# Performance work log

Hardware: AMD Instinct MI355X
Metric: run time of the kernel (lower is better)

Reference implementation:

```python
import jax, jax.numpy as jnp
import numpy as np

B, L, I, O, H = 128, 1024, 256, 256, 1024


def setup_inputs() -> dict:
    key = jax.random.key(0)
    ks = jax.random.split(key, 7)
    s = 1.0 / np.sqrt(H)  # torch LSTM/Linear init scale
    u = lambda k, shape: jax.random.uniform(k, shape, jnp.float32, -s, s)
    return {
        "trg": jax.random.normal(ks[0], (B, L, I), jnp.float32),
        "w_ih": u(ks[1], (4 * H, I)),
        "w_hh": u(ks[2], (4 * H, H)),
        "b_ih": u(ks[3], (4 * H,)),
        "b_hh": u(ks[4], (4 * H,)),
        "w_out": u(ks[5], (O, H)),
        "b_out": u(ks[6], (O,)),
    }


def reference(trg, w_ih, w_hh, b_ih, b_hh, w_out, b_out):
    # trg: [B, L, I] -> time-major [L, B, I]
    trg_t = jnp.transpose(trg, (1, 0, 2))
    # teacher_forcing_ratio = 1.0: step t consumes trg[t-1] (step 0 consumes trg[0])
    x_seq = jnp.concatenate([trg_t[:1], trg_t[:-1]], axis=0)  # [L, B, I]
    hdim = w_hh.shape[1]
    # precompute input-to-gate projection for all steps: [L, B, 4H]
    xp = jnp.einsum('lbi,gi->lbg', x_seq, w_ih) + b_ih + b_hh

    def step(carry, xp_t):
        h, c = carry
        z = xp_t + h @ w_hh.T  # [B, 4H]
        i_g, f_g, g_g, o_g = jnp.split(z, 4, axis=-1)  # torch gate order i,f,g,o
        c = jax.nn.sigmoid(f_g) * c + jax.nn.sigmoid(i_g) * jnp.tanh(g_g)
        h = jax.nn.sigmoid(o_g) * jnp.tanh(c)
        return (h, c), h

    bsz = trg.shape[0]
    h0 = jnp.zeros((bsz, hdim), trg.dtype)
    c0 = jnp.zeros((bsz, hdim), trg.dtype)
    _, hs = jax.lax.scan(step, (h0, c0), xp)  # hs: [L, B, H]
    out = jnp.einsum('lbh,oh->lbo', hs, w_out) + b_out  # [L, B, O]
    return jnp.transpose(out, (1, 0, 2))  # [B, L, O]
```

## Files before the change

kernel.cpp:

```cpp
#include <hip/hip_runtime.h>

#define LL 1024
#define NBLK 256
#define NTHR 512

typedef __attribute__((ext_vector_type(8))) __bf16 bf16x8;
typedef __attribute__((ext_vector_type(4))) __bf16 bf16x4;
typedef __attribute__((ext_vector_type(16))) float f32x16;

__device__ __bf16 g_trg[128 * 1024 * 256];
__device__ __bf16 g_wih[4096 * 256];
__device__ __bf16 g_whh[4096 * 1024];
__device__ __bf16 g_wout[256 * 1024];
__device__ __bf16 g_ring[(size_t)1024 * 4 * 32768];
__device__ unsigned int g_flag[1024 * 4 * 64 * 8];

__device__ __forceinline__ float sigm(float x) { return 1.f / (1.f + __expf(-x)); }
__device__ __forceinline__ float tanh_(float x) {
  x = fminf(fmaxf(x, -15.f), 15.f);
  float e = __expf(2.f * x);
  return (e - 1.f) / (e + 1.f);
}

__global__ void zero_flag() {
  int i = blockIdx.x * blockDim.x + threadIdx.x;
  g_flag[i] = 0u;
}

__global__ void cvt4(const float* __restrict__ s, __bf16* __restrict__ d, int n4) {
  int i = blockIdx.x * blockDim.x + threadIdx.x;
  if (i < n4) {
    float4 v = ((const float4*)s)[i];
    bf16x4 o;
    o[0] = (__bf16)v.x; o[1] = (__bf16)v.y; o[2] = (__bf16)v.z; o[3] = (__bf16)v.w;
    ((bf16x4*)d)[i] = o;
  }
}

__global__ __launch_bounds__(NTHR, 2) void lstm_persist(
    const float* __restrict__ b_ih, const float* __restrict__ b_hh)
{
  const int tid = threadIdx.x;
  const int lane = tid & 63;
  const int w = tid >> 6;
  const int gid = blockIdx.x;
  const int p = (gid & 7) >> 1;
  const int q = ((gid >> 3) << 1) | (gid & 1);
  const int m = lane & 31;
  const int khalf = (lane >> 5) << 3;

  __shared__ float zp[8][32][40];

  __builtin_amdgcn_fence(__ATOMIC_ACQUIRE, "agent");

  const int colb = (q << 4) + (m & 15);
  const int grow0 = ((m >> 4) << 10) + colb;
  const int grow1 = ((2 + (m >> 4)) << 10) + colb;

  bf16x8 bR0[8], bR1[8], bX0[2], bX1[2];
  #pragma unroll
  for (int s = 0; s < 8; ++s) {
    int k = (w << 7) + (s << 4) + khalf;
    bR0[s] = *(const bf16x8*)(g_whh + grow0 * 1024 + k);
    bR1[s] = *(const bf16x8*)(g_whh + grow1 * 1024 + k);
  }
  #pragma unroll
  for (int s = 0; s < 2; ++s) {
    int k = (w << 5) + (s << 4) + khalf;
    bX0[s] = *(const bf16x8*)(g_wih + grow0 * 256 + k);
    bX1[s] = *(const bf16x8*)(g_wih + grow1 * 256 + k);
  }

  const int em = tid >> 4;
  const int ej = tid & 15;
  const int hcol = (q << 4) + ej;
  float bias_i = b_ih[hcol]        + b_hh[hcol];
  float bias_f = b_ih[1024 + hcol] + b_hh[1024 + hcol];
  float bias_g = b_ih[2048 + hcol] + b_hh[2048 + hcol];
  float bias_o = b_ih[3072 + hcol] + b_hh[3072 + hcol];

  const int rc = (q << 1) + (ej >> 3);
  const int ejlo = ej & 7;

  const int wcol = ((m & 15) << 1) + (m >> 4);

  float cst = 0.f;
  f32x16 acc0, acc1;
  #pragma unroll
  for (int r = 0; r < 16; ++r) { acc0[r] = 0.f; acc1[r] = 0.f; }

  const size_t trgbase = (size_t)(((p << 5) + m) << 10);

  #pragma unroll 1
  for (int t = 0; t < LL; ++t) {
    {
      int tx = (t == 0) ? 0 : (t - 1);
      const __bf16* trow = g_trg + ((trgbase + tx) << 8);
      bf16x8 ax0 = *(const bf16x8*)(trow + (w << 5) + khalf);
      bf16x8 ax1 = *(const bf16x8*)(trow + (w << 5) + 16 + khalf);
      acc0 = __builtin_amdgcn_mfma_f32_32x32x16_bf16(ax0, bX0[0], acc0, 0, 0, 0);
      acc1 = __builtin_amdgcn_mfma_f32_32x32x16_bf16(ax0, bX1[0], acc1, 0, 0, 0);
      acc0 = __builtin_amdgcn_mfma_f32_32x32x16_bf16(ax1, bX0[1], acc0, 0, 0, 0);
      acc1 = __builtin_amdgcn_mfma_f32_32x32x16_bf16(ax1, bX1[1], acc1, 0, 0, 0);
    }
    if (t > 0) {
      unsigned int* fp = g_flag + ((((t - 1) << 2) + p) << 9) + (w << 6) + lane;
      unsigned f = __hip_atomic_load(fp, __ATOMIC_RELAXED, __HIP_MEMORY_SCOPE_AGENT);
      int spins = 0;
      while (__any(f == 0u)) {
        __builtin_amdgcn_s_sleep(1);
        f = __hip_atomic_load(fp, __ATOMIC_RELAXED, __HIP_MEMORY_SCOPE_AGENT);
        if (++spins > 30000) break;
      }
      const __bf16* rrd = g_ring + (size_t)(t - 1) * 131072 + (p << 15);
      #pragma unroll
      for (int s = 0; s < 8; ++s) {
        int k0 = (w << 7) + (s << 4);
        bf16x8 a = *(const bf16x8*)(rrd + ((k0 + khalf) << 5) + (m << 3));
        acc0 = __builtin_amdgcn_mfma_f32_32x32x16_bf16(a, bR0[s], acc0, 0, 0, 0);
        acc1 = __builtin_amdgcn_mfma_f32_32x32x16_bf16(a, bR1[s], acc1, 0, 0, 0);
      }
    }
    #pragma unroll
    for (int r = 0; r < 16; ++r) {
      int row = (r & 3) + ((r >> 2) << 3) + ((lane >> 5) << 2);
      zp[w][row][wcol] = acc0[r];  acc0[r] = 0.f;
    }
    __syncthreads();
    float zi = bias_i, zf = bias_f;
    #pragma unroll
    for (int s = 0; s < 8; ++s) {
      float2 v = *(const float2*)&zp[s][em][ej << 1];
      zi += v.x; zf += v.y;
    }
    __syncthreads();
    #pragma unroll
    for (int r = 0; r < 16; ++r) {
      int row = (r & 3) + ((r >> 2) << 3) + ((lane >> 5) << 2);
      zp[w][row][wcol] = acc1[r];  acc1[r] = 0.f;
    }
    float si = sigm(zi);
    float cp = sigm(zf) * cst;
    __syncthreads();
    float zg = bias_g, zo = bias_o;
    #pragma unroll
    for (int s = 0; s < 8; ++s) {
      float2 v = *(const float2*)&zp[s][em][ej << 1];
      zg += v.x; zo += v.y;
    }
    cst = cp + si * tanh_(zg);
    float h = sigm(zo) * tanh_(cst);
    {
      __bf16 hb = (__bf16)h;
      unsigned hu = (unsigned)*(unsigned short*)&hb;
      unsigned pu = (unsigned)__shfl_xor((int)hu, 1);
      if ((ej & 1) == 0) {
        unsigned word = hu | (pu << 16);
        unsigned* dst = (unsigned*)(g_ring + (size_t)t * 131072 + (p << 15))
                        + (rc << 7) + (em << 2) + (ejlo >> 1);
        __hip_atomic_store(dst, word, __ATOMIC_RELAXED, __HIP_MEMORY_SCOPE_AGENT);
      }
    }
    asm volatile("s_waitcnt vmcnt(0)" ::: "memory");
    if (lane == 0) {
      __hip_atomic_store(g_flag + (((t << 2) + p) << 9) + (q << 3) + w, 1u,
                         __ATOMIC_RELAXED, __HIP_MEMORY_SCOPE_AGENT);
    }
    __syncthreads();
  }
}

__global__ __launch_bounds__(NTHR, 2) void out_proj(
    const float* __restrict__ b_out, float* __restrict__ out)
{
  const int tid = threadIdx.x;
  const int lane = tid & 63;
  const int w = tid >> 6;
  const int m = lane & 31;
  const int khalf = (lane >> 5) << 3;
  const int gid = blockIdx.x;
  const int p = gid & 3;
  const int oc = (gid >> 2) & 7;
  const int tcb = gid >> 5;

  __shared__ float zp[8][32][36];

  bf16x8 bo[8];
  #pragma unroll
  for (int s = 0; s < 8; ++s)
    bo[s] = *(const bf16x8*)(g_wout + ((oc << 5) + m) * 1024 + (w << 7) + (s << 4) + khalf);

  const int em = tid >> 4;
  const int c  = tid & 15;
  const float ob0 = b_out[(oc << 5) + c];
  const float ob1 = b_out[(oc << 5) + 16 + c];

  const int t0 = tcb << 7;
  bf16x8 a[8], an[8];
  {
    const __bf16* rrd = g_ring + (size_t)t0 * 131072 + (p << 15);
    #pragma unroll
    for (int s = 0; s < 8; ++s)
      a[s] = *(const bf16x8*)(rrd + (((w << 7) + (s << 4) + khalf) << 5) + (m << 3));
  }

  #pragma unroll 1
  for (int ti = 0; ti < 128; ++ti) {
    const int t = t0 + ti;
    if (ti < 127) {
      const __bf16* rrd = g_ring + (size_t)(t + 1) * 131072 + (p << 15);
      #pragma unroll
      for (int s = 0; s < 8; ++s)
        an[s] = *(const bf16x8*)(rrd + (((w << 7) + (s << 4) + khalf) << 5) + (m << 3));
    }
    f32x16 acc;
    #pragma unroll
    for (int r = 0; r < 16; ++r) acc[r] = 0.f;
    #pragma unroll
    for (int s = 0; s < 8; ++s)
      acc = __builtin_amdgcn_mfma_f32_32x32x16_bf16(a[s], bo[s], acc, 0, 0, 0);
    #pragma unroll
    for (int r = 0; r < 16; ++r) {
      int row = (r & 3) + ((r >> 2) << 3) + ((lane >> 5) << 2);
      zp[w][row][m] = acc[r];
    }
    __syncthreads();
    float o0 = ob0, o1 = ob1;
    #pragma unroll
    for (int s = 0; s < 8; ++s) {
      o0 += zp[s][em][c];
      o1 += zp[s][em][16 + c];
    }
    float* orow = out + ((((size_t)((p << 5) + em) << 10) + t) << 8) + (oc << 5);
    orow[c]      = o0;
    orow[16 + c] = o1;
    __syncthreads();
    #pragma unroll
    for (int s = 0; s < 8; ++s) a[s] = an[s];
  }
}

extern "C" void kernel_launch(void* const* d_in, const int* in_sizes, int n_in,
                              void* d_out, int out_size, void* d_ws, size_t ws_size,
                              hipStream_t stream) {
  const float* trg   = (const float*)d_in[0];
  const float* w_ih  = (const float*)d_in[1];
  const float* w_hh  = (const float*)d_in[2];
  const float* b_ih  = (const float*)d_in[3];
  const float* b_hh  = (const float*)d_in[4];
  const float* w_out = (const float*)d_in[5];
  const float* b_out = (const float*)d_in[6];

  __bf16 *p_trg, *p_wih, *p_whh, *p_wout;
  hipGetSymbolAddress((void**)&p_trg,  HIP_SYMBOL(g_trg));
  hipGetSymbolAddress((void**)&p_wih,  HIP_SYMBOL(g_wih));
  hipGetSymbolAddress((void**)&p_whh,  HIP_SYMBOL(g_whh));
  hipGetSymbolAddress((void**)&p_wout, HIP_SYMBOL(g_wout));

  cvt4<<<dim3(33554432 / 4 / 256), dim3(256), 0, stream>>>(trg,   p_trg,  33554432 / 4);
  cvt4<<<dim3(1048576  / 4 / 256), dim3(256), 0, stream>>>(w_ih,  p_wih,  1048576  / 4);
  cvt4<<<dim3(4194304  / 4 / 256), dim3(256), 0, stream>>>(w_hh,  p_whh,  4194304  / 4);
  cvt4<<<dim3(262144   / 4 / 256), dim3(256), 0, stream>>>(w_out, p_wout, 262144   / 4);
  zero_flag<<<dim3(8192), dim3(256), 0, stream>>>();

  lstm_persist<<<dim3(NBLK), dim3(NTHR), 0, stream>>>(b_ih, b_hh);
  out_proj<<<dim3(NBLK), dim3(NTHR), 0, stream>>>(b_out, (float*)d_out);
}
```

Measured before the change: 4.387 ms.

## Aggregate per-block sync flags and merge gate reductions into one LDS pass

Each workgroup now publishes a single global flag, set by the last wave to finish via an LDS atomic counter, instead of one flag per wave. Only wave 0 polls the 64 producer flags and then releases the other waves through an LDS generation word. The gate partial sums for both accumulators go into one wider LDS buffer, which removes two of the four barriers per step. This cuts global flag traffic and barrier count on the serial recurrence path. The cost is one extra intra-block hop, busy-spinning waves without sleep, and 72KB of dynamic LDS, which may limit occupancy to 2 blocks per CU.

```diff
diff --git a/kernel.cpp b/kernel.cpp
--- a/kernel.cpp
+++ b/kernel.cpp
@@ -3,6 +3,7 @@
 #define LL 1024
 #define NBLK 256
 #define NTHR 512
+#define SMEM_BYTES (73728 + 8)
 
 typedef __attribute__((ext_vector_type(8))) __bf16 bf16x8;
 typedef __attribute__((ext_vector_type(4))) __bf16 bf16x4;
@@ -13,7 +14,7 @@
 __device__ __bf16 g_whh[4096 * 1024];
 __device__ __bf16 g_wout[256 * 1024];
 __device__ __bf16 g_ring[(size_t)1024 * 4 * 32768];
-__device__ unsigned int g_flag[1024 * 4 * 64 * 8];
+__device__ unsigned int g_flag[1024 * 4 * 64];
 
 __device__ __forceinline__ float sigm(float x) { return 1.f / (1.f + __expf(-x)); }
 __device__ __forceinline__ float tanh_(float x) {
@@ -40,6 +41,10 @@
 __global__ __launch_bounds__(NTHR, 2) void lstm_persist(
     const float* __restrict__ b_ih, const float* __restrict__ b_hh)
 {
+  extern __shared__ __align__(16) char smem[];
+  float (*zp)[32][72] = (float (*)[32][72])smem;
+  unsigned* ctrl = (unsigned*)(smem + 73728);
+
   const int tid = threadIdx.x;
   const int lane = tid & 63;
   const int w = tid >> 6;
@@ -49,9 +54,9 @@
   const int m = lane & 31;
   const int khalf = (lane >> 5) << 3;
 
-  __shared__ float zp[8][32][40];
-
   __builtin_amdgcn_fence(__ATOMIC_ACQUIRE, "agent");
+
+  if (tid < 2) ctrl[tid] = 0u;
 
   const int colb = (q << 4) + (m & 15);
   const int grow0 = ((m >> 4) << 10) + colb;
@@ -90,6 +95,7 @@
   for (int r = 0; r < 16; ++r) { acc0[r] = 0.f; acc1[r] = 0.f; }
 
   const size_t trgbase = (size_t)(((p << 5) + m) << 10);
+  __syncthreads();
 
   #pragma unroll 1
   for (int t = 0; t < LL; ++t) {
@@ -104,14 +110,23 @@
       acc1 = __builtin_amdgcn_mfma_f32_32x32x16_bf16(ax1, bX1[1], acc1, 0, 0, 0);
     }
     if (t > 0) {
-      unsigned int* fp = g_flag + ((((t - 1) << 2) + p) << 9) + (w << 6) + lane;
-      unsigned f = __hip_atomic_load(fp, __ATOMIC_RELAXED, __HIP_MEMORY_SCOPE_AGENT);
-      int spins = 0;
-      while (__any(f == 0u)) {
-        __builtin_amdgcn_s_sleep(1);
-        f = __hip_atomic_load(fp, __ATOMIC_RELAXED, __HIP_MEMORY_SCOPE_AGENT);
-        if (++spins > 30000) break;
-      }
+      if (w == 0) {
+        unsigned int* fp = g_flag + ((((t - 1) << 2) + p) << 6) + lane;
+        unsigned f = __hip_atomic_load(fp, __ATOMIC_RELAXED, __HIP_MEMORY_SCOPE_AGENT);
+        int spins = 0;
+        while (__any(f == 0u)) {
+          f = __hip_atomic_load(fp, __ATOMIC_RELAXED, __HIP_MEMORY_SCOPE_AGENT);
+          if (++spins > 2000000) break;
+        }
+        ((volatile unsigned*)ctrl)[1] = (unsigned)t;
+      } else {
+        volatile unsigned* gp = ((volatile unsigned*)ctrl) + 1;
+        int spins = 0;
+        while (*gp < (unsigned)t) {
+          if (++spins > 200000000) break;
+        }
+      }
+      asm volatile("" ::: "memory");
       const __bf16* rrd = g_ring + (size_t)(t - 1) * 131072 + (p << 15);
       #pragma unroll
       for (int s = 0; s < 8; ++s) {
@@ -124,33 +139,21 @@
     #pragma unroll
     for (int r = 0; r < 16; ++r) {
       int row = (r & 3) + ((r >> 2) << 3) + ((lane >> 5) << 2);
-      zp[w][row][wcol] = acc0[r];  acc0[r] = 0.f;
-    }
-    __syncthreads();
-    float zi = bias_i, zf = bias_f;
-    #pragma unroll
-    for (int s = 0; s < 8; ++s) {
-      float2 v = *(const float2*)&zp[s][em][ej << 1];
-      zi += v.x; zf += v.y;
-    }
-    __syncthreads();
-    #pragma unroll
-    for (int r = 0; r < 16; ++r) {
-      int row = (r & 3) + ((r >> 2) << 3) + ((lane >> 5) << 2);
-      zp[w][row][wcol] = acc1[r];  acc1[r] = 0.f;
-    }
-    float si = sigm(zi);
-    float cp = sigm(zf) * cst;
-    __syncthreads();
-    float zg = bias_g, zo = bias_o;
-    #pragma unroll
-    for (int s = 0; s < 8; ++s) {
-      float2 v = *(const float2*)&zp[s][em][ej << 1];
-      zg += v.x; zo += v.y;
-    }
-    cst = cp + si * tanh_(zg);
-    float h = sigm(zo) * tanh_(cst);
+      zp[w][row][wcol]      = acc0[r];  acc0[r] = 0.f;
+      zp[w][row][32 + wcol] = acc1[r];  acc1[r] = 0.f;
+    }
+    __syncthreads();
+
     {
+      float zi = bias_i, zf = bias_f, zg = bias_g, zo = bias_o;
+      #pragma unroll
+      for (int s = 0; s < 8; ++s) {
+        float2 v0 = *(const float2*)&zp[s][em][ej << 1];
+        float2 v1 = *(const float2*)&zp[s][em][32 + (ej << 1)];
+        zi += v0.x; zf += v0.y; zg += v1.x; zo += v1.y;
+      }
+      cst = sigm(zf) * cst + sigm(zi) * tanh_(zg);
+      float h = sigm(zo) * tanh_(cst);
       __bf16 hb = (__bf16)h;
       unsigned hu = (unsigned)*(unsigned short*)&hb;
       unsigned pu = (unsigned)__shfl_xor((int)hu, 1);
@@ -163,8 +166,11 @@
     }
     asm volatile("s_waitcnt vmcnt(0)" ::: "memory");
     if (lane == 0) {
-      __hip_atomic_store(g_flag + (((t << 2) + p) << 9) + (q << 3) + w, 1u,
-                         __ATOMIC_RELAXED, __HIP_MEMORY_SCOPE_AGENT);
+      unsigned old = atomicAdd(&ctrl[0], 1u);
+      if (old == (unsigned)((t << 3) + 7)) {
+        __hip_atomic_store(g_flag + (((t << 2) + p) << 6) + q, 1u,
+                           __ATOMIC_RELAXED, __HIP_MEMORY_SCOPE_AGENT);
+      }
     }
     __syncthreads();
   }
@@ -251,6 +257,13 @@
   const float* w_out = (const float*)d_in[5];
   const float* b_out = (const float*)d_in[6];
 
+  static int attr_set = 0;
+  if (!attr_set) {
+    hipFuncSetAttribute((const void*)lstm_persist,
+                        hipFuncAttributeMaxDynamicSharedMemorySize, SMEM_BYTES);
+    attr_set = 1;
+  }
+
   __bf16 *p_trg, *p_wih, *p_whh, *p_wout;
   hipGetSymbolAddress((void**)&p_trg,  HIP_SYMBOL(g_trg));
   hipGetSymbolAddress((void**)&p_wih,  HIP_SYMBOL(g_wih));
@@ -261,8 +274,8 @@
   cvt4<<<dim3(1048576  / 4 / 256), dim3(256), 0, stream>>>(w_ih,  p_wih,  1048576  / 4);
   cvt4<<<dim3(4194304  / 4 / 256), dim3(256), 0, stream>>>(w_hh,  p_whh,  4194304  / 4);
   cvt4<<<dim3(262144   / 4 / 256), dim3(256), 0, stream>>>(w_out, p_wout, 262144   / 4);
-  zero_flag<<<dim3(8192), dim3(256), 0, stream>>>();
-
-  lstm_persist<<<dim3(NBLK), dim3(NTHR), 0, stream>>>(b_ih, b_hh);
+  zero_flag<<<dim3(1024), dim3(256), 0, stream>>>();
+
+  lstm_persist<<<dim3(NBLK), dim3(NTHR), SMEM_BYTES, stream>>>(b_ih, b_hh);
   out_proj<<<dim3(NBLK), dim3(NTHR), 0, stream>>>(b_out, (float*)d_out);
 }
```

After: 4.662 ms. +6.3%, slower.
